# Kernel optimization log

Hardware: AMD Instinct MI355X
Metric: run time of the kernel (lower is better)

## Reference

```python
import jax, jax.numpy as jnp
import numpy as np

IMAGE_SIZE = 256  # init kwarg image_size
BS, NCAM, N = 2, 3, 128


def _normalise_scale_factor(v):
    v = v / v.mean()
    sf = 0.2 / jnp.abs(v - 1.0).max()
    return jnp.where(sf < 1.0, (v - 1.0) * sf + 1.0, v)


def setup_inputs() -> dict:
    key = jax.random.key(0)
    ks = jax.random.split(key, 7)
    S = IMAGE_SIZE
    # 2D projected points in pixel coords [0, S)
    points = jax.random.uniform(ks[0], (BS, NCAM, N, 2), dtype=jnp.float32) * S
    # per-point render params in the model's clamp ranges
    sigmas = jax.random.uniform(ks[1], (BS, N), dtype=jnp.float32) * 0.06 + 0.041
    exponents = jax.random.uniform(ks[2], (BS, N), dtype=jnp.float32) * 1.5 + 0.5
    intensities = jax.random.uniform(ks[3], (BS, N), dtype=jnp.float32) * 0.6 + 0.41
    # per-camera scale factors near 1
    camera_sigmas = jax.random.uniform(ks[4], (BS, NCAM), dtype=jnp.float32) * 0.2 + 0.9
    camera_exponents = jax.random.uniform(ks[5], (BS, NCAM), dtype=jnp.float32) * 0.2 + 0.9
    camera_intensities = jax.random.uniform(ks[6], (BS, NCAM), dtype=jnp.float32) * 0.2 + 0.9
    return {
        'points': points, 'sigmas': sigmas, 'exponents': exponents,
        'intensities': intensities, 'camera_sigmas': camera_sigmas,
        'camera_exponents': camera_exponents, 'camera_intensities': camera_intensities,
    }


def reference(points, sigmas, exponents, intensities,
              camera_sigmas, camera_exponents, camera_intensities):
    S = IMAGE_SIZE
    bs, N = points.shape[0], points.shape[2]
    s2 = S // 2
    # normalise pixel coords to [-1, 1], flatten cameras into batch
    p = jnp.clip((points - s2) / s2, -1.0, 1.0).reshape(bs * 3, N, 2)
    # camera scale factors (normalised as in forward())
    cs = _normalise_scale_factor(camera_sigmas).reshape(bs * 3)
    ce = _normalise_scale_factor(camera_exponents).reshape(bs * 3)
    ci = _normalise_scale_factor(camera_intensities).reshape(bs * 3)
    # repeat_interleave(3, 0) over batch -> (bs*3, N, 1, 1)
    sig = (jnp.repeat(sigmas, 3, axis=0) * cs[:, None])[:, :, None, None]
    expn = (jnp.repeat(exponents, 3, axis=0) * ce[:, None])[:, :, None, None]
    inten = (jnp.repeat(intensities, 3, axis=0) * ci[:, None])[:, :, None, None]
    grid = jnp.linspace(-1.0, 1.0, S, dtype=jnp.float32)
    px = p[:, :, 0][:, :, None, None]  # (bs3, N, 1, 1)
    py = p[:, :, 1][:, :, None, None]
    # squared distance of every point to every pixel: (bs3, N, S, S)
    # y varies over axis -2 (rows), x over axis -1 (cols), matching meshgrid(ij)
    dst = (grid[None, None, None, :] - px) ** 2 + (grid[None, None, :, None] - py) ** 2
    blobs = jnp.exp(-(dst / (2.0 * sig ** 2)) ** expn)
    masks = jnp.minimum((blobs * inten).max(axis=1), 1.0)  # amax over N points
    masks = masks.reshape(bs, 3, S, S)
    blobs = blobs.reshape(bs, 3, N, S, S)
    return masks, blobs
```

## Files before the change

### kernel.cpp

```cpp
#include <hip/hip_runtime.h>

#define SZ   256
#define NPTS 128
#define NB3  6

#define EXP2F(x) __builtin_amdgcn_exp2f(x)
#define LOG2F(x) __builtin_amdgcn_logf(x)

__device__ __forceinline__ float norm6(const float* __restrict__ v, int idx) {
    float a0 = v[0], a1 = v[1], a2 = v[2], a3 = v[3], a4 = v[4], a5 = v[5];
    float mean = (a0 + a1 + a2 + a3 + a4 + a5) * (1.0f / 6.0f);
    float inv = 1.0f / mean;
    float b0 = a0 * inv, b1 = a1 * inv, b2 = a2 * inv;
    float b3 = a3 * inv, b4 = a4 * inv, b5 = a5 * inv;
    float d = fmaxf(fmaxf(fmaxf(fabsf(b0 - 1.f), fabsf(b1 - 1.f)),
                          fmaxf(fabsf(b2 - 1.f), fabsf(b3 - 1.f))),
                    fmaxf(fabsf(b4 - 1.f), fabsf(b5 - 1.f)));
    float sf = 0.2f / d;
    float vi = v[idx] * inv;
    return (sf < 1.0f) ? (vi - 1.0f) * sf + 1.0f : vi;
}

__global__ __launch_bounds__(256) void render_kernel(
    const float* __restrict__ points,
    const float* __restrict__ sigmas,
    const float* __restrict__ exponents,
    const float* __restrict__ intensities,
    const float* __restrict__ cam_s,
    const float* __restrict__ cam_e,
    const float* __restrict__ cam_i,
    float* __restrict__ masks,
    float* __restrict__ blobs)
{
    __shared__ float4 s_p[NPTS];
    __shared__ float  s_i[NPTS];

    const int b3  = blockIdx.x >> 8;
    const int y   = blockIdx.x & 255;
    const int tid = threadIdx.x;

    if (tid < NPTS) {
        const int b = b3 / 3;
        const float cs = norm6(cam_s, b3);
        const float ce = norm6(cam_e, b3);
        const float ci = norm6(cam_i, b3);
        float px = points[(b3 * NPTS + tid) * 2 + 0];
        float py = points[(b3 * NPTS + tid) * 2 + 1];
        px = fminf(fmaxf((px - 128.0f) * (1.0f / 128.0f), -1.0f), 1.0f);
        py = fminf(fmaxf((py - 128.0f) * (1.0f / 128.0f), -1.0f), 1.0f);
        const float sg = sigmas[b * NPTS + tid] * cs;
        const float e  = exponents[b * NPTS + tid] * ce;
        const float q  = 1.0f / (2.0f * sg * sg);
        const float C  = 0.5287663729448977f;
        const float c2 = fmaf(e, LOG2F(q), C);
        s_p[tid] = make_float4(px, py, e, c2);
        s_i[tid] = intensities[b * NPTS + tid] * ci;
    }
    __syncthreads();

    const float gy = -1.0f + (float)y   * (2.0f / 255.0f);
    const float gx = -1.0f + (float)tid * (2.0f / 255.0f);

    float m = 0.0f;
    float* bptr = blobs + (size_t)b3 * NPTS * SZ * SZ + (size_t)y * SZ + tid;

    #pragma unroll 4
    for (int n = 0; n < NPTS; ++n) {
        const float4 p = s_p[n];
        const float dx = gx - p.x;
        const float dy = gy - p.y;
        const float u  = fmaf(dx, dx, dy * dy);
        const float l  = fmaf(p.z, LOG2F(u), p.w);
        const float t  = EXP2F(l);
        const float bl = EXP2F(-t);
        bptr[(size_t)n * (SZ * SZ)] = bl;
        m = fmaxf(m, bl * s_i[n]);
    }

    masks[(size_t)b3 * SZ * SZ + (size_t)y * SZ + tid] = fminf(m, 1.0f);
}

extern "C" void kernel_launch(void* const* d_in, const int* in_sizes, int n_in,
                              void* d_out, int out_size, void* d_ws, size_t ws_size,
                              hipStream_t stream) {
    const float* points      = (const float*)d_in[0];
    const float* sigmas      = (const float*)d_in[1];
    const float* exponents   = (const float*)d_in[2];
    const float* intensities = (const float*)d_in[3];
    const float* cam_s       = (const float*)d_in[4];
    const float* cam_e       = (const float*)d_in[5];
    const float* cam_i       = (const float*)d_in[6];

    float* out   = (float*)d_out;
    float* masks = out;
    float* blobs = out + NB3 * SZ * SZ;

    hipLaunchKernelGGL(render_kernel, dim3(NB3 * SZ), dim3(256), 0, stream,
                       points, sigmas, exponents, intensities,
                       cam_s, cam_e, cam_i, masks, blobs);
}
```

Before: 207.4 us.

## Split kernel into mask blocks and per-plane blob blocks with float4 stores

Splits the single kernel into two block roles: mask blocks that compute the per-pixel max without writing blobs, and blob blocks that each own a 16-row slab of one point's plane and write it with float4 stores. The blob output (about 200 MB) becomes contiguous per block with vectorized writes instead of strided scalar stores spread across 128 planes. The cost is computing the blob values twice, once for masks and once for blobs, plus many more blocks that each redo the per-point parameter setup.

```diff
diff --git a/kernel.cpp b/kernel.cpp
--- a/kernel.cpp
+++ b/kernel.cpp
@@ -6,6 +6,10 @@
 
 #define EXP2F(x) __builtin_amdgcn_exp2f(x)
 #define LOG2F(x) __builtin_amdgcn_logf(x)
+
+#define MASK_BLOCKS  (NB3 * SZ)
+#define ROWS_PER_BLK 16
+#define BLOB_BLOCKS  (NB3 * NPTS * (SZ / ROWS_PER_BLK))
 
 __device__ __forceinline__ float norm6(const float* __restrict__ v, int idx) {
     float a0 = v[0], a1 = v[1], a2 = v[2], a3 = v[3], a4 = v[4], a5 = v[5];
@@ -32,52 +36,94 @@
     float* __restrict__ masks,
     float* __restrict__ blobs)
 {
-    __shared__ float4 s_p[NPTS];
-    __shared__ float  s_i[NPTS];
+    const int bid = blockIdx.x;
+    const int tid = threadIdx.x;
+    const float C = 0.5287663729448977f;
 
-    const int b3  = blockIdx.x >> 8;
-    const int y   = blockIdx.x & 255;
-    const int tid = threadIdx.x;
+    if (bid < MASK_BLOCKS) {
+        __shared__ float4 s_p[NPTS];
+        __shared__ float  s_i[NPTS];
+        const int b3 = bid >> 8;
+        const int y  = bid & 255;
 
-    if (tid < NPTS) {
-        const int b = b3 / 3;
+        if (tid < NPTS) {
+            const int b = b3 / 3;
+            const float cs = norm6(cam_s, b3);
+            const float ce = norm6(cam_e, b3);
+            const float ci = norm6(cam_i, b3);
+            float px = points[(b3 * NPTS + tid) * 2 + 0];
+            float py = points[(b3 * NPTS + tid) * 2 + 1];
+            px = fminf(fmaxf((px - 128.0f) * (1.0f / 128.0f), -1.0f), 1.0f);
+            py = fminf(fmaxf((py - 128.0f) * (1.0f / 128.0f), -1.0f), 1.0f);
+            const float sg = sigmas[b * NPTS + tid] * cs;
+            const float e  = exponents[b * NPTS + tid] * ce;
+            const float q  = 1.0f / (2.0f * sg * sg);
+            s_p[tid] = make_float4(px, py, e, fmaf(e, LOG2F(q), C));
+            s_i[tid] = intensities[b * NPTS + tid] * ci;
+        }
+        __syncthreads();
+
+        const float gy = -1.0f + (float)y   * (2.0f / 255.0f);
+        const float gx = -1.0f + (float)tid * (2.0f / 255.0f);
+
+        float m = 0.0f;
+        #pragma unroll 4
+        for (int n = 0; n < NPTS; ++n) {
+            const float4 p = s_p[n];
+            const float dx = gx - p.x;
+            const float dy = gy - p.y;
+            const float u  = fmaf(dx, dx, dy * dy);
+            const float t  = EXP2F(fmaf(p.z, LOG2F(u), p.w));
+            const float bl = EXP2F(-t);
+            m = fmaxf(m, bl * s_i[n]);
+        }
+        masks[(size_t)b3 * SZ * SZ + (size_t)y * SZ + tid] = fminf(m, 1.0f);
+    } else {
+        const int pid   = bid - MASK_BLOCKS;
+        const int plane = pid >> 4;
+        const int r0    = (pid & 15) * ROWS_PER_BLK;
+        const int b3    = plane >> 7;
+        const int n     = plane & 127;
+        const int b     = b3 / 3;
+
         const float cs = norm6(cam_s, b3);
         const float ce = norm6(cam_e, b3);
-        const float ci = norm6(cam_i, b3);
-        float px = points[(b3 * NPTS + tid) * 2 + 0];
-        float py = points[(b3 * NPTS + tid) * 2 + 1];
+        float px = points[(b3 * NPTS + n) * 2 + 0];
+        float py = points[(b3 * NPTS + n) * 2 + 1];
         px = fminf(fmaxf((px - 128.0f) * (1.0f / 128.0f), -1.0f), 1.0f);
         py = fminf(fmaxf((py - 128.0f) * (1.0f / 128.0f), -1.0f), 1.0f);
-        const float sg = sigmas[b * NPTS + tid] * cs;
-        const float e  = exponents[b * NPTS + tid] * ce;
+        const float sg = sigmas[b * NPTS + n] * cs;
+        const float e  = exponents[b * NPTS + n] * ce;
         const float q  = 1.0f / (2.0f * sg * sg);
-        const float C  = 0.5287663729448977f;
         const float c2 = fmaf(e, LOG2F(q), C);
-        s_p[tid] = make_float4(px, py, e, c2);
-        s_i[tid] = intensities[b * NPTS + tid] * ci;
+
+        const int wave = tid >> 6;
+        const int x0   = (tid & 63) << 2;
+        const float gx0 = -1.0f + (float)(x0    ) * (2.0f / 255.0f);
+        const float gx1 = -1.0f + (float)(x0 + 1) * (2.0f / 255.0f);
+        const float gx2 = -1.0f + (float)(x0 + 2) * (2.0f / 255.0f);
+        const float gx3 = -1.0f + (float)(x0 + 3) * (2.0f / 255.0f);
+        const float d0 = gx0 - px, d1 = gx1 - px, d2 = gx2 - px, d3 = gx3 - px;
+        const float dx20 = d0 * d0, dx21 = d1 * d1;
+        const float dx22 = d2 * d2, dx23 = d3 * d3;
+
+        const int row0 = r0 + wave * 4;
+        float* base = blobs + (size_t)plane * (SZ * SZ) + (size_t)row0 * SZ + x0;
+
+        #pragma unroll
+        for (int i = 0; i < 4; ++i) {
+            const float gy  = -1.0f + (float)(row0 + i) * (2.0f / 255.0f);
+            const float dy  = gy - py;
+            const float dy2 = dy * dy;
+            const float u0 = dx20 + dy2, u1 = dx21 + dy2;
+            const float u2 = dx22 + dy2, u3 = dx23 + dy2;
+            const float bl0 = EXP2F(-EXP2F(fmaf(e, LOG2F(u0), c2)));
+            const float bl1 = EXP2F(-EXP2F(fmaf(e, LOG2F(u1), c2)));
+            const float bl2 = EXP2F(-EXP2F(fmaf(e, LOG2F(u2), c2)));
+            const float bl3 = EXP2F(-EXP2F(fmaf(e, LOG2F(u3), c2)));
+            *((float4*)(base + (size_t)i * SZ)) = make_float4(bl0, bl1, bl2, bl3);
+        }
     }
-    __syncthreads();
-
-    const float gy = -1.0f + (float)y   * (2.0f / 255.0f);
-    const float gx = -1.0f + (float)tid * (2.0f / 255.0f);
-
-    float m = 0.0f;
-    float* bptr = blobs + (size_t)b3 * NPTS * SZ * SZ + (size_t)y * SZ + tid;
-
-    #pragma unroll 4
-    for (int n = 0; n < NPTS; ++n) {
-        const float4 p = s_p[n];
-        const float dx = gx - p.x;
-        const float dy = gy - p.y;
-        const float u  = fmaf(dx, dx, dy * dy);
-        const float l  = fmaf(p.z, LOG2F(u), p.w);
-        const float t  = EXP2F(l);
-        const float bl = EXP2F(-t);
-        bptr[(size_t)n * (SZ * SZ)] = bl;
-        m = fmaxf(m, bl * s_i[n]);
-    }
-
-    masks[(size_t)b3 * SZ * SZ + (size_t)y * SZ + tid] = fminf(m, 1.0f);
 }
 
 extern "C" void kernel_launch(void* const* d_in, const int* in_sizes, int n_in,
@@ -95,7 +141,8 @@
     float* masks = out;
     float* blobs = out + NB3 * SZ * SZ;
 
-    hipLaunchKernelGGL(render_kernel, dim3(NB3 * SZ), dim3(256), 0, stream,
+    hipLaunchKernelGGL(render_kernel, dim3(MASK_BLOCKS + BLOB_BLOCKS), dim3(256),
+                       0, stream,
                        points, sigmas, exponents, intensities,
                        cam_s, cam_e, cam_i, masks, blobs);
 }
```

Result: slower. 224.4 us (+8.2%).
